# Optimization experiments

Measured on AMD Instinct MI355X. Metric: run time of the kernel, lower is better.

Reference implementation:

```python
import jax, jax.numpy as jnp
import numpy as np

B, S, D, H = 2, 2048, 1024, 16
HD = D // H  # head_dim = 64

def setup_inputs() -> dict:
    key = jax.random.key(0)
    ks = jax.random.split(key, 10)
    s = 1.0 / np.sqrt(D)
    return {
        "hidden_states": jax.random.normal(ks[0], (B, S, D), jnp.float32),
        "attention_mask": jnp.ones((B, S), jnp.float32),
        "q_w": jax.random.uniform(ks[1], (D, D), jnp.float32, -s, s),
        "q_b": jax.random.uniform(ks[2], (D,), jnp.float32, -s, s),
        "k_w": jax.random.uniform(ks[3], (D, D), jnp.float32, -s, s),
        "k_b": jax.random.uniform(ks[4], (D,), jnp.float32, -s, s),
        "v_w": jax.random.uniform(ks[5], (D, D), jnp.float32, -s, s),
        "v_b": jax.random.uniform(ks[6], (D,), jnp.float32, -s, s),
        "o_w": jax.random.uniform(ks[7], (D, D), jnp.float32, -s, s),
        "o_b": jax.random.uniform(ks[8], (D,), jnp.float32, -s, s),
    }

def reference(hidden_states, attention_mask, q_w, q_b, k_w, k_b, v_w, v_b, o_w, o_b):
    scale = HD ** -0.5
    # projections; torch Linear: x @ W^T + b. Here weights stored as (D, D) used directly.
    q = hidden_states @ q_w + q_b  # [B,S,D]
    k = hidden_states @ k_w + k_b
    v = hidden_states @ v_w + v_b
    # split heads -> [B,H,S,HD]
    q = q.reshape(B, S, H, HD).transpose(0, 2, 1, 3)
    k = k.reshape(B, S, H, HD).transpose(0, 2, 1, 3)
    v = v.reshape(B, S, H, HD).transpose(0, 2, 1, 3)
    scores = jnp.einsum('bhqd,bhkd->bhqk', q, k) * scale  # [B,H,S,S]
    # additive mask from 2D [B,S] mask (1=keep, 0=mask)
    scores = scores + (1.0 - attention_mask)[:, None, None, :] * -10000.0
    attn = jax.nn.softmax(scores, axis=-1)
    ctx = jnp.einsum('bhqk,bhkd->bhqd', attn, v)  # [B,H,S,HD]
    ctx = ctx.transpose(0, 2, 1, 3).reshape(B, S, D)
    return ctx @ o_w + o_b
```

## Files before the change

kernel.cpp:

```cpp
#include <hip/hip_runtime.h>
#include <hip/hip_bf16.h>

#define B_ 2
#define S_ 2048
#define D_ 1024
#define H_ 16
#define HD_ 64

#define QSCALE 0.18033688f
#define MLOG2E 14426.950408f

#define EXP2(x) __builtin_amdgcn_exp2f(x)

typedef __attribute__((ext_vector_type(8))) short bf16x8;
typedef __attribute__((ext_vector_type(4))) short short4v;
typedef __attribute__((ext_vector_type(4))) float floatx4;
typedef __attribute__((ext_vector_type(16))) float f32x16;

static __device__ __forceinline__ float bf2f(short u) {
  union { float f; unsigned int i; } c;
  c.i = ((unsigned int)(unsigned short)u) << 16;
  return c.f;
}
static __device__ __forceinline__ short f2bf(float f) {
  union { float f; unsigned int i; } c; c.f = f;
  unsigned int r = c.i + 0x7FFFu + ((c.i >> 16) & 1u);
  return (short)(r >> 16);
}

static __device__ __forceinline__ int cvtpk_bf16(float a, float b) {
  int r;
  asm("v_cvt_pk_bf16_f32 %0, %1, %2" : "=v"(r) : "v"(a), "v"(b));
  return r;
}
static __device__ __forceinline__ void swap32(int& a, int& b) {
  asm("v_permlane32_swap_b32 %0, %1" : "+v"(a), "+v"(b));
}

static __device__ __forceinline__ void gld_lds16(const void* g, void* l) {
  __builtin_amdgcn_global_load_lds(
      (const __attribute__((address_space(1))) unsigned int*)g,
      (__attribute__((address_space(3))) unsigned int*)l, 16, 0, 0);
}

__global__ __launch_bounds__(256)
void prep(const float* __restrict__ w0, const float* __restrict__ w1,
          const float* __restrict__ w2, const float* __restrict__ w3,
          const float* __restrict__ hs, short* __restrict__ WT,
          short* __restrict__ Xb) {
  const int z = blockIdx.z;
  if (z < 4) {
    __shared__ short t[64][65];
    const float* src = z == 0 ? w0 : z == 1 ? w1 : z == 2 ? w2 : w3;
    short* dst = WT + (size_t)z * D_ * D_;
    const int tx = threadIdx.x & 63, ty = threadIdx.x >> 6;
    const int r0 = blockIdx.y * 64, c0 = blockIdx.x * 64;
    for (int r = ty; r < 64; r += 4)
      t[r][tx] = f2bf(src[(size_t)(r0 + r) * D_ + c0 + tx]);
    __syncthreads();
    for (int r = ty; r < 64; r += 4)
      dst[(size_t)(c0 + r) * D_ + r0 + tx] = t[tx][r];
  } else {
    const int bid = blockIdx.y * 16 + blockIdx.x;
    const float4* in4 = (const float4*)hs;
    short4v* out4 = (short4v*)Xb;
#pragma unroll
    for (int i = 0; i < 16; i++) {
      const int idx = bid * 4096 + i * 256 + threadIdx.x;
      const float4 v = in4[idx];
      short4v o;
      o[0] = f2bf(v.x); o[1] = f2bf(v.y); o[2] = f2bf(v.z); o[3] = f2bf(v.w);
      out4[idx] = o;
    }
  }
}

__global__ __launch_bounds__(256, 2)
void gemm_qkv(const short* __restrict__ X, const short* __restrict__ WT,
              const float* __restrict__ qb, const float* __restrict__ kb,
              const float* __restrict__ vb,
              short* __restrict__ Qo, short* __restrict__ Ko,
              short* __restrict__ Vt) {
  __shared__ __align__(16) short As[128 * 32];
  __shared__ __align__(16) short Bs[128 * 32];
  const int tid = threadIdx.x;
  const int wave = tid >> 6, lane = tid & 63;
  const int col = lane & 15, quad = lane >> 4;
  const int m0 = blockIdx.x * 128;
  const int nt = blockIdx.y;
  const int widx = nt >> 3;
  const int n1 = (nt & 7) * 128;
  const short* Bsrc = WT + (size_t)widx * D_ * D_ + (size_t)n1 * D_;
  const int b = m0 >> 11;

  const int srow = tid >> 2;
  const int skcol = (tid & 3) * 8;
  const short* ga = X + (size_t)(m0 + srow) * D_ + skcol;
  const short* gb = Bsrc + (size_t)srow * D_ + skcol;
  short* la = As + tid * 8;
  short* lb = Bs + tid * 8;

  floatx4 acc[4][4];
#pragma unroll
  for (int i = 0; i < 4; i++)
#pragma unroll
    for (int j = 0; j < 4; j++) acc[i][j] = floatx4{0.f, 0.f, 0.f, 0.f};

  if (widx < 2) {
    const int wseq = (wave >> 1) * 64;
    const int wfeat = (wave & 1) * 64;
    for (int k0 = 0; k0 < D_; k0 += 32) {
      gld_lds16(ga, la);
      gld_lds16(ga + 64 * D_, la + 2048);
      gld_lds16(gb, lb);
      gld_lds16(gb + 64 * D_, lb + 2048);
      ga += 32; gb += 32;
      __syncthreads();
      bf16x8 xf[4], wf[4];
#pragma unroll
      for (int j = 0; j < 4; j++)
        xf[j] = *(const bf16x8*)(As + (wseq + j * 16 + col) * 32 + quad * 8);
#pragma unroll
      for (int i = 0; i < 4; i++)
        wf[i] = *(const bf16x8*)(Bs + (wfeat + i * 16 + col) * 32 + quad * 8);
#pragma unroll
      for (int i = 0; i < 4; i++)
#pragma unroll
        for (int j = 0; j < 4; j++)
          acc[i][j] = __builtin_amdgcn_mfma_f32_16x16x32_bf16(wf[i], xf[j],
                                                              acc[i][j], 0, 0, 0);
      __syncthreads();
    }
    const float* bias = widx == 0 ? qb : kb;
    short* dst = widx == 0 ? Qo : Ko;
    const float scale = widx == 0 ? QSCALE : 1.0f;
#pragma unroll
    for (int i = 0; i < 4; i++) {
      const int nf = n1 + wfeat + i * 16 + quad * 4;
      const int h = nf >> 6, hd = nf & 63;
      const float4 bv = *(const float4*)(bias + nf);
#pragma unroll
      for (int j = 0; j < 4; j++) {
        const int s = (m0 + wseq + j * 16 + col) & (S_ - 1);
        short4v pk;
        pk[0] = f2bf((acc[i][j][0] + bv.x) * scale);
        pk[1] = f2bf((acc[i][j][1] + bv.y) * scale);
        pk[2] = f2bf((acc[i][j][2] + bv.z) * scale);
        pk[3] = f2bf((acc[i][j][3] + bv.w) * scale);
        *(short4v*)(dst + ((size_t)(b * H_ + h) * S_ + s) * HD_ + hd) = pk;
      }
    }
  } else {
    const int wrow = (wave & 1) * 64;
    const int wcol = (wave >> 1) * 64;
    for (int k0 = 0; k0 < D_; k0 += 32) {
      gld_lds16(ga, la);
      gld_lds16(ga + 64 * D_, la + 2048);
      gld_lds16(gb, lb);
      gld_lds16(gb + 64 * D_, lb + 2048);
      ga += 32; gb += 32;
      __syncthreads();
      bf16x8 af[4], bfr[4];
#pragma unroll
      for (int i = 0; i < 4; i++)
        af[i] = *(const bf16x8*)(As + (wrow + i * 16 + col) * 32 + quad * 8);
#pragma unroll
      for (int j = 0; j < 4; j++)
        bfr[j] = *(const bf16x8*)(Bs + (wcol + j * 16 + col) * 32 + quad * 8);
#pragma unroll
      for (int i = 0; i < 4; i++)
#pragma unroll
        for (int j = 0; j < 4; j++)
          acc[i][j] = __builtin_amdgcn_mfma_f32_16x16x32_bf16(af[i], bfr[j],
                                                              acc[i][j], 0, 0, 0);
      __syncthreads();
    }
    float bv[4];
#pragma unroll
    for (int j = 0; j < 4; j++) bv[j] = vb[n1 + wcol + j * 16 + col];
#pragma unroll
    for (int i = 0; i < 4; i++) {
      const int s = (m0 + wrow + i * 16 + quad * 4) & (S_ - 1);
#pragma unroll
      for (int j = 0; j < 4; j++) {
        const int nl = n1 + wcol + j * 16 + col;
        const int h = nl >> 6, hd = nl & 63;
        short4v pk;
#pragma unroll
        for (int r = 0; r < 4; r++) pk[r] = f2bf(acc[i][j][r] + bv[j]);
        *(short4v*)(Vt + ((size_t)(b * H_ + h) * HD_ + hd) * S_ + s) = pk;
      }
    }
  }
}

__global__ __launch_bounds__(256, 2)
void attn(const short* __restrict__ Q, const short* __restrict__ K,
          const short* __restrict__ Vt, const float* __restrict__ mask,
          short* __restrict__ ctx) {
  __shared__ __align__(16) short Ks[2][4096];
  __shared__ __align__(16) short Vs[2][4096];
  __shared__ __align__(16) float Wb[S_];
  const int tid = threadIdx.x, wave = tid >> 6, lane = tid & 63;
  const int l31 = lane & 31, hi = lane >> 5, x7 = l31 & 7;
  const int lin = blockIdx.x;
  const int qt = (lin >> 3) & 15;
  const int gi = (lin & 7) + ((lin >> 7) << 3);
  const int h = gi & 15, b = gi >> 4;
  const short* Qh = Q + (size_t)(b * H_ + h) * S_ * HD_;
  const short* Kh = K + (size_t)(b * H_ + h) * S_ * HD_;
  const short* Vh = Vt + (size_t)(b * H_ + h) * HD_ * S_;
  const float* mk = mask + (size_t)b * S_;
  const int q0 = qt * 128 + wave * 32;

  const int r1 = tid >> 3, c1 = (tid & 7) ^ (r1 & 7);
  const int r2 = r1 + 32,  c2 = (tid & 7) ^ (r2 & 7);

  gld_lds16(Kh + (size_t)r1 * HD_ + c1 * 8, &Ks[0][tid * 8]);
  gld_lds16(Kh + (size_t)r2 * HD_ + c2 * 8, &Ks[0][(tid + 256) * 8]);
  gld_lds16(Vh + (size_t)r1 * S_ + c1 * 8, &Vs[0][tid * 8]);
  gld_lds16(Vh + (size_t)r2 * S_ + c2 * 8, &Vs[0][(tid + 256) * 8]);

  for (int i = tid; i < S_; i += 256)
    Wb[i] = (mk[i] - 1.0f) * MLOG2E;

  bf16x8 qf[4];
  {
    const short* qp = Qh + (size_t)(q0 + l31) * HD_ + hi * 8;
#pragma unroll
    for (int c = 0; c < 4; c++) qf[c] = *(const bf16x8*)(qp + c * 16);
  }

  bf16x8 ones;
#pragma unroll
  for (int i = 0; i < 8; i++) ones[i] = (short)0x3F80;

  f32x16 acc0, acc1, rsa;
#pragma unroll
  for (int r = 0; r < 16; r++) { acc0[r] = 0.f; acc1[r] = 0.f; rsa[r] = 0.f; }

  const int kbase = l31 * 64;
  int ko[4];
#pragma unroll
  for (int c = 0; c < 4; c++) ko[c] = ((((c << 1) | hi) ^ x7) << 3);

  __syncthreads();

  for (int it = 0; it < S_ / 64; it++) {
    const int buf = it & 1;
    const int kt = it * 64;
    if (it + 1 < S_ / 64) {
      const int kn = kt + 64;
      gld_lds16(Kh + (size_t)(kn + r1) * HD_ + c1 * 8, &Ks[buf ^ 1][tid * 8]);
      gld_lds16(Kh + (size_t)(kn + r2) * HD_ + c2 * 8, &Ks[buf ^ 1][(tid + 256) * 8]);
      gld_lds16(Vh + (size_t)r1 * S_ + kn + c1 * 8, &Vs[buf ^ 1][tid * 8]);
      gld_lds16(Vh + (size_t)r2 * S_ + kn + c2 * 8, &Vs[buf ^ 1][(tid + 256) * 8]);
    }

    bf16x8 pB[4];
#pragma unroll
    for (int t = 0; t < 2; t++) {
      const int kb2 = kt + t * 32 + 4 * hi;
      const float4 b0 = *(const float4*)&Wb[kb2];
      const float4 b1 = *(const float4*)&Wb[kb2 + 8];
      const float4 b2 = *(const float4*)&Wb[kb2 + 16];
      const float4 b3 = *(const float4*)&Wb[kb2 + 24];
      f32x16 z;
      z[0] = b0.x; z[1] = b0.y; z[2]  = b0.z; z[3]  = b0.w;
      z[4] = b1.x; z[5] = b1.y; z[6]  = b1.z; z[7]  = b1.w;
      z[8] = b2.x; z[9] = b2.y; z[10] = b2.z; z[11] = b2.w;
      z[12] = b3.x; z[13] = b3.y; z[14] = b3.z; z[15] = b3.w;
      const short* kp = &Ks[buf][t * 2048 + kbase];
#pragma unroll
      for (int c = 0; c < 4; c++) {
        const bf16x8 kf = *(const bf16x8*)(kp + ko[c]);
        z = __builtin_amdgcn_mfma_f32_32x32x16_bf16(kf, qf[c], z, 0, 0, 0);
      }
      float p[16];
#pragma unroll
      for (int r = 0; r < 16; r++) p[r] = EXP2(z[r]);
      int a0 = cvtpk_bf16(p[0], p[1]),   a1 = cvtpk_bf16(p[2], p[3]);
      int cc0 = cvtpk_bf16(p[4], p[5]),  cc1 = cvtpk_bf16(p[6], p[7]);
      int e0 = cvtpk_bf16(p[8], p[9]),   e1 = cvtpk_bf16(p[10], p[11]);
      int g0 = cvtpk_bf16(p[12], p[13]), g1 = cvtpk_bf16(p[14], p[15]);
      swap32(a0, cc0); swap32(a1, cc1);
      swap32(e0, g0);  swap32(e1, g1);
      union { int i[4]; bf16x8 v; } u0, u1;
      u0.i[0] = a0; u0.i[1] = a1; u0.i[2] = cc0; u0.i[3] = cc1;
      u1.i[0] = e0; u1.i[1] = e1; u1.i[2] = g0;  u1.i[3] = g1;
      pB[t * 2] = u0.v;
      pB[t * 2 + 1] = u1.v;
    }

#pragma unroll
    for (int kc = 0; kc < 4; kc++)
      rsa = __builtin_amdgcn_mfma_f32_32x32x16_bf16(ones, pB[kc], rsa, 0, 0, 0);

    const short* vp0 = &Vs[buf][kbase];
    const short* vp1 = &Vs[buf][2048 + kbase];
#pragma unroll
    for (int kc = 0; kc < 4; kc++) {
      const bf16x8 vf0 = *(const bf16x8*)(vp0 + ko[kc]);
      const bf16x8 vf1 = *(const bf16x8*)(vp1 + ko[kc]);
      acc0 = __builtin_amdgcn_mfma_f32_32x32x16_bf16(vf0, pB[kc], acc0, 0, 0, 0);
      acc1 = __builtin_amdgcn_mfma_f32_32x32x16_bf16(vf1, pB[kc], acc1, 0, 0, 0);
    }
    __syncthreads();
  }

  const float inv = 1.0f / (rsa[0] + 1e-30f);
  const size_t row = (size_t)b * S_ + q0 + l31;
#pragma unroll
  for (int g4 = 0; g4 < 4; g4++) {
    short4v o0, o1;
#pragma unroll
    for (int j = 0; j < 4; j++) {
      o0[j] = f2bf(acc0[g4 * 4 + j] * inv);
      o1[j] = f2bf(acc1[g4 * 4 + j] * inv);
    }
    short* cp = ctx + row * D_ + h * HD_ + g4 * 8 + 4 * hi;
    *(short4v*)(cp) = o0;
    *(short4v*)(cp + 32) = o1;
  }
}

__global__ __launch_bounds__(256, 2)
void gemm_out(const short* __restrict__ X, const short* __restrict__ WT,
              const float* __restrict__ ob, float* __restrict__ out) {
  __shared__ __align__(16) short As[64 * 32];
  __shared__ __align__(16) short Bs[128 * 32];
  const int tid = threadIdx.x;
  const int wave = tid >> 6, lane = tid & 63;
  const int col = lane & 15, quad = lane >> 4;
  const int m0 = blockIdx.x * 64;
  const int n0 = blockIdx.y * 128;
  const short* Bsrc = WT + (size_t)n0 * D_;
  const int wrow = (wave & 1) * 32;
  const int wcol = (wave >> 1) * 64;

  floatx4 acc[2][4];
#pragma unroll
  for (int i = 0; i < 2; i++)
#pragma unroll
    for (int j = 0; j < 4; j++) acc[i][j] = floatx4{0.f, 0.f, 0.f, 0.f};

  const int arow = tid >> 2, akcol = (tid & 3) * 8;
  const short* ga = X + (size_t)(m0 + arow) * D_ + akcol;
  const short* gb = Bsrc + (size_t)arow * D_ + akcol;
  short* la = As + tid * 8;
  short* lb = Bs + tid * 8;

  for (int k0 = 0; k0 < D_; k0 += 32) {
    gld_lds16(ga, la);
    gld_lds16(gb, lb);
    gld_lds16(gb + 64 * D_, lb + 2048);
    ga += 32; gb += 32;
    __syncthreads();
    bf16x8 af[2], bfr[4];
#pragma unroll
    for (int i = 0; i < 2; i++)
      af[i] = *(const bf16x8*)(As + (wrow + i * 16 + col) * 32 + quad * 8);
#pragma unroll
    for (int j = 0; j < 4; j++)
      bfr[j] = *(const bf16x8*)(Bs + (wcol + j * 16 + col) * 32 + quad * 8);
#pragma unroll
    for (int i = 0; i < 2; i++)
#pragma unroll
      for (int j = 0; j < 4; j++)
        acc[i][j] = __builtin_amdgcn_mfma_f32_16x16x32_bf16(af[i], bfr[j],
                                                            acc[i][j], 0, 0, 0);
    __syncthreads();
  }

  float bv[4];
#pragma unroll
  for (int j = 0; j < 4; j++) bv[j] = ob[n0 + wcol + j * 16 + col];

#pragma unroll
  for (int i = 0; i < 2; i++) {
    const int m = m0 + wrow + i * 16 + quad * 4;
#pragma unroll
    for (int j = 0; j < 4; j++) {
      const int n = n0 + wcol + j * 16 + col;
#pragma unroll
      for (int r = 0; r < 4; r++)
        out[(size_t)(m + r) * D_ + n] = acc[i][j][r] + bv[j];
    }
  }
}

extern "C" void kernel_launch(void* const* d_in, const int* in_sizes, int n_in,
                              void* d_out, int out_size, void* d_ws, size_t ws_size,
                              hipStream_t stream) {
  (void)in_sizes; (void)n_in; (void)out_size; (void)ws_size;
  const float* hs  = (const float*)d_in[0];
  const float* msk = (const float*)d_in[1];
  const float* qw  = (const float*)d_in[2];
  const float* qb  = (const float*)d_in[3];
  const float* kw  = (const float*)d_in[4];
  const float* kb  = (const float*)d_in[5];
  const float* vw  = (const float*)d_in[6];
  const float* vb  = (const float*)d_in[7];
  const float* ow  = (const float*)d_in[8];
  const float* ob  = (const float*)d_in[9];
  float* out = (float*)d_out;
  char* ws = (char*)d_ws;

  short* Xb  = (short*)(ws);
  short* WT  = (short*)(ws + (8ull  << 20));
  short* Qp  = (short*)(ws + (16ull << 20));
  short* Kp  = (short*)(ws + (24ull << 20));
  short* Vtp = (short*)(ws + (32ull << 20));
  short* Ctx = Xb;

  prep<<<dim3(16, 16, 5), 256, 0, stream>>>(qw, kw, vw, ow, hs, WT, Xb);
  gemm_qkv<<<dim3(32, 24), 256, 0, stream>>>(Xb, WT, qb, kb, vb, Qp, Kp, Vtp);
  attn<<<dim3(512), 256, 0, stream>>>(Qp, Kp, Vtp, msk, Ctx);
  gemm_out<<<dim3(64, 8), 256, 0, stream>>>(Ctx, WT + 3ull * D_ * D_, ob, out);
}
```

Measured before the change: 195.5 us.

## Shrink attention blocks to two waves, stagger KV start, add MFMA priority

```diff
diff --git a/kernel.cpp b/kernel.cpp
--- a/kernel.cpp
+++ b/kernel.cpp
@@ -17,11 +17,6 @@
 typedef __attribute__((ext_vector_type(4))) float floatx4;
 typedef __attribute__((ext_vector_type(16))) float f32x16;
 
-static __device__ __forceinline__ float bf2f(short u) {
-  union { float f; unsigned int i; } c;
-  c.i = ((unsigned int)(unsigned short)u) << 16;
-  return c.f;
-}
 static __device__ __forceinline__ short f2bf(float f) {
   union { float f; unsigned int i; } c; c.f = f;
   unsigned int r = c.i + 0x7FFFu + ((c.i >> 16) & 1u);
@@ -194,35 +189,38 @@
   }
 }
 
-__global__ __launch_bounds__(256, 2)
+__global__ __launch_bounds__(128, 2)
 void attn(const short* __restrict__ Q, const short* __restrict__ K,
           const short* __restrict__ Vt, const float* __restrict__ mask,
           short* __restrict__ ctx) {
   __shared__ __align__(16) short Ks[2][4096];
   __shared__ __align__(16) short Vs[2][4096];
-  __shared__ __align__(16) float Wb[S_];
   const int tid = threadIdx.x, wave = tid >> 6, lane = tid & 63;
   const int l31 = lane & 31, hi = lane >> 5, x7 = l31 & 7;
   const int lin = blockIdx.x;
-  const int qt = (lin >> 3) & 15;
-  const int gi = (lin & 7) + ((lin >> 7) << 3);
+  const int qt = (lin >> 3) & 31;
+  const int gi = (lin & 7) | ((lin >> 8) << 3);
   const int h = gi & 15, b = gi >> 4;
   const short* Qh = Q + (size_t)(b * H_ + h) * S_ * HD_;
   const short* Kh = K + (size_t)(b * H_ + h) * S_ * HD_;
   const short* Vh = Vt + (size_t)(b * H_ + h) * HD_ * S_;
   const float* mk = mask + (size_t)b * S_;
-  const int q0 = qt * 128 + wave * 32;
-
-  const int r1 = tid >> 3, c1 = (tid & 7) ^ (r1 & 7);
-  const int r2 = r1 + 32,  c2 = (tid & 7) ^ (r2 & 7);
-
-  gld_lds16(Kh + (size_t)r1 * HD_ + c1 * 8, &Ks[0][tid * 8]);
-  gld_lds16(Kh + (size_t)r2 * HD_ + c2 * 8, &Ks[0][(tid + 256) * 8]);
-  gld_lds16(Vh + (size_t)r1 * S_ + c1 * 8, &Vs[0][tid * 8]);
-  gld_lds16(Vh + (size_t)r2 * S_ + c2 * 8, &Vs[0][(tid + 256) * 8]);
-
-  for (int i = tid; i < S_; i += 256)
-    Wb[i] = (mk[i] - 1.0f) * MLOG2E;
+  const int q0 = qt * 64 + wave * 32;
+
+  int srow[4], schk[4];
+#pragma unroll
+  for (int i = 0; i < 4; i++) {
+    const int s = tid + i * 128;
+    srow[i] = s >> 3;
+    schk[i] = ((s & 7) ^ (srow[i] & 7)) * 8;
+  }
+
+  const int kt0 = qt * 64;
+#pragma unroll
+  for (int i = 0; i < 4; i++) {
+    gld_lds16(Kh + (size_t)(kt0 + srow[i]) * HD_ + schk[i], &Ks[0][(tid + i * 128) * 8]);
+    gld_lds16(Vh + (size_t)srow[i] * S_ + kt0 + schk[i], &Vs[0][(tid + i * 128) * 8]);
+  }
 
   bf16x8 qf[4];
   {
@@ -248,34 +246,43 @@
 
   for (int it = 0; it < S_ / 64; it++) {
     const int buf = it & 1;
-    const int kt = it * 64;
+    const int kt = ((it + qt) & 31) * 64;
     if (it + 1 < S_ / 64) {
-      const int kn = kt + 64;
-      gld_lds16(Kh + (size_t)(kn + r1) * HD_ + c1 * 8, &Ks[buf ^ 1][tid * 8]);
-      gld_lds16(Kh + (size_t)(kn + r2) * HD_ + c2 * 8, &Ks[buf ^ 1][(tid + 256) * 8]);
-      gld_lds16(Vh + (size_t)r1 * S_ + kn + c1 * 8, &Vs[buf ^ 1][tid * 8]);
-      gld_lds16(Vh + (size_t)r2 * S_ + kn + c2 * 8, &Vs[buf ^ 1][(tid + 256) * 8]);
+      const int kn = ((it + 1 + qt) & 31) * 64;
+#pragma unroll
+      for (int i = 0; i < 4; i++) {
+        gld_lds16(Kh + (size_t)(kn + srow[i]) * HD_ + schk[i],
+                  &Ks[buf ^ 1][(tid + i * 128) * 8]);
+        gld_lds16(Vh + (size_t)srow[i] * S_ + kn + schk[i],
+                  &Vs[buf ^ 1][(tid + i * 128) * 8]);
+      }
     }
 
     bf16x8 pB[4];
 #pragma unroll
     for (int t = 0; t < 2; t++) {
       const int kb2 = kt + t * 32 + 4 * hi;
-      const float4 b0 = *(const float4*)&Wb[kb2];
-      const float4 b1 = *(const float4*)&Wb[kb2 + 8];
-      const float4 b2 = *(const float4*)&Wb[kb2 + 16];
-      const float4 b3 = *(const float4*)&Wb[kb2 + 24];
+      const float4 b0 = *(const float4*)&mk[kb2];
+      const float4 b1 = *(const float4*)&mk[kb2 + 8];
+      const float4 b2 = *(const float4*)&mk[kb2 + 16];
+      const float4 b3 = *(const float4*)&mk[kb2 + 24];
       f32x16 z;
-      z[0] = b0.x; z[1] = b0.y; z[2]  = b0.z; z[3]  = b0.w;
-      z[4] = b1.x; z[5] = b1.y; z[6]  = b1.z; z[7]  = b1.w;
-      z[8] = b2.x; z[9] = b2.y; z[10] = b2.z; z[11] = b2.w;
-      z[12] = b3.x; z[13] = b3.y; z[14] = b3.z; z[15] = b3.w;
+      z[0]  = (b0.x - 1.0f) * MLOG2E; z[1]  = (b0.y - 1.0f) * MLOG2E;
+      z[2]  = (b0.z - 1.0f) * MLOG2E; z[3]  = (b0.w - 1.0f) * MLOG2E;
+      z[4]  = (b1.x - 1.0f) * MLOG2E; z[5]  = (b1.y - 1.0f) * MLOG2E;
+      z[6]  = (b1.z - 1.0f) * MLOG2E; z[7]  = (b1.w - 1.0f) * MLOG2E;
+      z[8]  = (b2.x - 1.0f) * MLOG2E; z[9]  = (b2.y - 1.0f) * MLOG2E;
+      z[10] = (b2.z - 1.0f) * MLOG2E; z[11] = (b2.w - 1.0f) * MLOG2E;
+      z[12] = (b3.x - 1.0f) * MLOG2E; z[13] = (b3.y - 1.0f) * MLOG2E;
+      z[14] = (b3.z - 1.0f) * MLOG2E; z[15] = (b3.w - 1.0f) * MLOG2E;
       const short* kp = &Ks[buf][t * 2048 + kbase];
+      __builtin_amdgcn_s_setprio(1);
 #pragma unroll
       for (int c = 0; c < 4; c++) {
         const bf16x8 kf = *(const bf16x8*)(kp + ko[c]);
         z = __builtin_amdgcn_mfma_f32_32x32x16_bf16(kf, qf[c], z, 0, 0, 0);
       }
+      __builtin_amdgcn_s_setprio(0);
       float p[16];
 #pragma unroll
       for (int r = 0; r < 16; r++) p[r] = EXP2(z[r]);
@@ -292,12 +299,12 @@
       pB[t * 2 + 1] = u1.v;
     }
 
+    const short* vp0 = &Vs[buf][kbase];
+    const short* vp1 = &Vs[buf][2048 + kbase];
+    __builtin_amdgcn_s_setprio(1);
 #pragma unroll
     for (int kc = 0; kc < 4; kc++)
       rsa = __builtin_amdgcn_mfma_f32_32x32x16_bf16(ones, pB[kc], rsa, 0, 0, 0);
-
-    const short* vp0 = &Vs[buf][kbase];
-    const short* vp1 = &Vs[buf][2048 + kbase];
 #pragma unroll
     for (int kc = 0; kc < 4; kc++) {
       const bf16x8 vf0 = *(const bf16x8*)(vp0 + ko[kc]);
@@ -305,6 +312,7 @@
       acc0 = __builtin_amdgcn_mfma_f32_32x32x16_bf16(vf0, pB[kc], acc0, 0, 0, 0);
       acc1 = __builtin_amdgcn_mfma_f32_32x32x16_bf16(vf1, pB[kc], acc1, 0, 0, 0);
     }
+    __builtin_amdgcn_s_setprio(0);
     __syncthreads();
   }
 
@@ -415,6 +423,6 @@
 
   prep<<<dim3(16, 16, 5), 256, 0, stream>>>(qw, kw, vw, ow, hs, WT, Xb);
   gemm_qkv<<<dim3(32, 24), 256, 0, stream>>>(Xb, WT, qb, kb, vb, Qp, Kp, Vtp);
-  attn<<<dim3(512), 256, 0, stream>>>(Qp, Kp, Vtp, msk, Ctx);
+  attn<<<dim3(1024), 128, 0, stream>>>(Qp, Kp, Vtp, msk, Ctx);
   gemm_out<<<dim3(64, 8), 256, 0, stream>>>(Ctx, WT + 3ull * D_ * D_, ob, out);
 }
```

Result: slower. 206.6 us (+5.7%).

## Split attention KV range in two and add a combine kernel

Applied to the files above, without the earlier changes.

```diff
diff --git a/kernel.cpp b/kernel.cpp
--- a/kernel.cpp
+++ b/kernel.cpp
@@ -17,11 +17,6 @@
 typedef __attribute__((ext_vector_type(4))) float floatx4;
 typedef __attribute__((ext_vector_type(16))) float f32x16;
 
-static __device__ __forceinline__ float bf2f(short u) {
-  union { float f; unsigned int i; } c;
-  c.i = ((unsigned int)(unsigned short)u) << 16;
-  return c.f;
-}
 static __device__ __forceinline__ short f2bf(float f) {
   union { float f; unsigned int i; } c; c.f = f;
   unsigned int r = c.i + 0x7FFFu + ((c.i >> 16) & 1u);
@@ -194,35 +189,46 @@
   }
 }
 
-__global__ __launch_bounds__(256, 2)
+__global__ __launch_bounds__(256, 4)
 void attn(const short* __restrict__ Q, const short* __restrict__ K,
           const short* __restrict__ Vt, const float* __restrict__ mask,
-          short* __restrict__ ctx) {
+          float* __restrict__ ctxP0, float* __restrict__ ctxP1,
+          float* __restrict__ rsP0, float* __restrict__ rsP1) {
   __shared__ __align__(16) short Ks[2][4096];
   __shared__ __align__(16) short Vs[2][4096];
-  __shared__ __align__(16) float Wb[S_];
+  __shared__ __align__(16) float Wb[1024];
   const int tid = threadIdx.x, wave = tid >> 6, lane = tid & 63;
   const int l31 = lane & 31, hi = lane >> 5, x7 = l31 & 7;
   const int lin = blockIdx.x;
-  const int qt = (lin >> 3) & 15;
-  const int gi = (lin & 7) + ((lin >> 7) << 3);
+  const int kh = (lin >> 3) & 1;
+  const int qt = (lin >> 4) & 15;
+  const int gi = (lin & 7) + ((lin >> 8) << 3);
   const int h = gi & 15, b = gi >> 4;
   const short* Qh = Q + (size_t)(b * H_ + h) * S_ * HD_;
   const short* Kh = K + (size_t)(b * H_ + h) * S_ * HD_;
   const short* Vh = Vt + (size_t)(b * H_ + h) * HD_ * S_;
   const float* mk = mask + (size_t)b * S_;
   const int q0 = qt * 128 + wave * 32;
-
-  const int r1 = tid >> 3, c1 = (tid & 7) ^ (r1 & 7);
-  const int r2 = r1 + 32,  c2 = (tid & 7) ^ (r2 & 7);
-
-  gld_lds16(Kh + (size_t)r1 * HD_ + c1 * 8, &Ks[0][tid * 8]);
-  gld_lds16(Kh + (size_t)r2 * HD_ + c2 * 8, &Ks[0][(tid + 256) * 8]);
-  gld_lds16(Vh + (size_t)r1 * S_ + c1 * 8, &Vs[0][tid * 8]);
-  gld_lds16(Vh + (size_t)r2 * S_ + c2 * 8, &Vs[0][(tid + 256) * 8]);
-
-  for (int i = tid; i < S_; i += 256)
-    Wb[i] = (mk[i] - 1.0f) * MLOG2E;
+  const int kk0 = kh * 1024;
+
+  int srow[2], schk[2];
+#pragma unroll
+  for (int i = 0; i < 2; i++) {
+    const int s = tid + i * 256;
+    srow[i] = s >> 3;
+    schk[i] = ((s & 7) ^ (srow[i] & 7)) * 8;
+  }
+
+#pragma unroll
+  for (int i = 0; i < 2; i++) {
+    gld_lds16(Kh + (size_t)(kk0 + srow[i]) * HD_ + schk[i],
+              &Ks[0][(tid + i * 256) * 8]);
+    gld_lds16(Vh + (size_t)srow[i] * S_ + kk0 + schk[i],
+              &Vs[0][(tid + i * 256) * 8]);
+  }
+
+  for (int i = tid; i < 1024; i += 256)
+    Wb[i] = (mk[kk0 + i] - 1.0f) * MLOG2E;
 
   bf16x8 qf[4];
   {
@@ -246,21 +252,24 @@
 
   __syncthreads();
 
-  for (int it = 0; it < S_ / 64; it++) {
+  for (int it = 0; it < 16; it++) {
     const int buf = it & 1;
-    const int kt = it * 64;
-    if (it + 1 < S_ / 64) {
-      const int kn = kt + 64;
-      gld_lds16(Kh + (size_t)(kn + r1) * HD_ + c1 * 8, &Ks[buf ^ 1][tid * 8]);
-      gld_lds16(Kh + (size_t)(kn + r2) * HD_ + c2 * 8, &Ks[buf ^ 1][(tid + 256) * 8]);
-      gld_lds16(Vh + (size_t)r1 * S_ + kn + c1 * 8, &Vs[buf ^ 1][tid * 8]);
-      gld_lds16(Vh + (size_t)r2 * S_ + kn + c2 * 8, &Vs[buf ^ 1][(tid + 256) * 8]);
+    const int ktl = it * 64;
+    if (it + 1 < 16) {
+      const int kn = kk0 + ktl + 64;
+#pragma unroll
+      for (int i = 0; i < 2; i++) {
+        gld_lds16(Kh + (size_t)(kn + srow[i]) * HD_ + schk[i],
+                  &Ks[buf ^ 1][(tid + i * 256) * 8]);
+        gld_lds16(Vh + (size_t)srow[i] * S_ + kn + schk[i],
+                  &Vs[buf ^ 1][(tid + i * 256) * 8]);
+      }
     }
 
     bf16x8 pB[4];
 #pragma unroll
     for (int t = 0; t < 2; t++) {
-      const int kb2 = kt + t * 32 + 4 * hi;
+      const int kb2 = ktl + t * 32 + 4 * hi;
       const float4 b0 = *(const float4*)&Wb[kb2];
       const float4 b1 = *(const float4*)&Wb[kb2 + 8];
       const float4 b2 = *(const float4*)&Wb[kb2 + 16];
@@ -271,11 +280,13 @@
       z[8] = b2.x; z[9] = b2.y; z[10] = b2.z; z[11] = b2.w;
       z[12] = b3.x; z[13] = b3.y; z[14] = b3.z; z[15] = b3.w;
       const short* kp = &Ks[buf][t * 2048 + kbase];
+      __builtin_amdgcn_s_setprio(1);
 #pragma unroll
       for (int c = 0; c < 4; c++) {
         const bf16x8 kf = *(const bf16x8*)(kp + ko[c]);
         z = __builtin_amdgcn_mfma_f32_32x32x16_bf16(kf, qf[c], z, 0, 0, 0);
       }
+      __builtin_amdgcn_s_setprio(0);
       float p[16];
 #pragma unroll
       for (int r = 0; r < 16; r++) p[r] = EXP2(z[r]);
@@ -292,12 +303,12 @@
       pB[t * 2 + 1] = u1.v;
     }
 
+    const short* vp0 = &Vs[buf][kbase];
+    const short* vp1 = &Vs[buf][2048 + kbase];
+    __builtin_amdgcn_s_setprio(1);
 #pragma unroll
     for (int kc = 0; kc < 4; kc++)
       rsa = __builtin_amdgcn_mfma_f32_32x32x16_bf16(ones, pB[kc], rsa, 0, 0, 0);
-
-    const short* vp0 = &Vs[buf][kbase];
-    const short* vp1 = &Vs[buf][2048 + kbase];
 #pragma unroll
     for (int kc = 0; kc < 4; kc++) {
       const bf16x8 vf0 = *(const bf16x8*)(vp0 + ko[kc]);
@@ -305,23 +316,51 @@
       acc0 = __builtin_amdgcn_mfma_f32_32x32x16_bf16(vf0, pB[kc], acc0, 0, 0, 0);
       acc1 = __builtin_amdgcn_mfma_f32_32x32x16_bf16(vf1, pB[kc], acc1, 0, 0, 0);
     }
+    __builtin_amdgcn_s_setprio(0);
     __syncthreads();
   }
 
-  const float inv = 1.0f / (rsa[0] + 1e-30f);
+  float* ctxP = kh ? ctxP1 : ctxP0;
+  float* rsP  = kh ? rsP1  : rsP0;
   const size_t row = (size_t)b * S_ + q0 + l31;
 #pragma unroll
   for (int g4 = 0; g4 < 4; g4++) {
-    short4v o0, o1;
-#pragma unroll
-    for (int j = 0; j < 4; j++) {
-      o0[j] = f2bf(acc0[g4 * 4 + j] * inv);
-      o1[j] = f2bf(acc1[g4 * 4 + j] * inv);
-    }
-    short* cp = ctx + row * D_ + h * HD_ + g4 * 8 + 4 * hi;
-    *(short4v*)(cp) = o0;
-    *(short4v*)(cp + 32) = o1;
-  }
+    float* cp = ctxP + row * D_ + h * HD_ + g4 * 8 + 4 * hi;
+    *(float4*)(cp) = make_float4(acc0[g4 * 4 + 0], acc0[g4 * 4 + 1],
+                                 acc0[g4 * 4 + 2], acc0[g4 * 4 + 3]);
+    *(float4*)(cp + 32) = make_float4(acc1[g4 * 4 + 0], acc1[g4 * 4 + 1],
+                                      acc1[g4 * 4 + 2], acc1[g4 * 4 + 3]);
+  }
+  if (hi == 0)
+    rsP[(size_t)(b * H_ + h) * S_ + q0 + l31] = rsa[0];
+}
+
+__global__ __launch_bounds__(256)
+void combine(const float* __restrict__ P0, const float* __restrict__ P1,
+             const float* __restrict__ rs0, const float* __restrict__ rs1,
+             short* __restrict__ ctx) {
+  const int t = blockIdx.x * 256 + threadIdx.x;
+  const int row = t >> 7;
+  const int dq = (t & 127) * 8;
+  const int b = row >> 11, s = row & (S_ - 1);
+  const int h = dq >> 6;
+  const size_t base = (size_t)row * D_ + dq;
+  const float4 a0 = *(const float4*)(P0 + base);
+  const float4 a1 = *(const float4*)(P0 + base + 4);
+  const float4 c0 = *(const float4*)(P1 + base);
+  const float4 c1 = *(const float4*)(P1 + base + 4);
+  const size_t ri = (size_t)(b * H_ + h) * S_ + s;
+  const float inv = 1.0f / (rs0[ri] + rs1[ri] + 1e-30f);
+  union { short sh[8]; int4 v; } o;
+  o.sh[0] = f2bf((a0.x + c0.x) * inv);
+  o.sh[1] = f2bf((a0.y + c0.y) * inv);
+  o.sh[2] = f2bf((a0.z + c0.z) * inv);
+  o.sh[3] = f2bf((a0.w + c0.w) * inv);
+  o.sh[4] = f2bf((a1.x + c1.x) * inv);
+  o.sh[5] = f2bf((a1.y + c1.y) * inv);
+  o.sh[6] = f2bf((a1.z + c1.z) * inv);
+  o.sh[7] = f2bf((a1.w + c1.w) * inv);
+  *(int4*)(ctx + base) = o.v;
 }
 
 __global__ __launch_bounds__(256, 2)
@@ -406,15 +445,20 @@
   float* out = (float*)d_out;
   char* ws = (char*)d_ws;
 
-  short* Xb  = (short*)(ws);
-  short* WT  = (short*)(ws + (8ull  << 20));
-  short* Qp  = (short*)(ws + (16ull << 20));
-  short* Kp  = (short*)(ws + (24ull << 20));
-  short* Vtp = (short*)(ws + (32ull << 20));
-  short* Ctx = Xb;
+  short* Xb   = (short*)(ws);
+  short* WT   = (short*)(ws + (8ull  << 20));
+  short* Qp   = (short*)(ws + (16ull << 20));
+  short* Kp   = (short*)(ws + (24ull << 20));
+  short* Vtp  = (short*)(ws + (32ull << 20));
+  float* ctxP0 = (float*)(ws + (40ull << 20));
+  float* ctxP1 = (float*)(ws + (56ull << 20));
+  float* rsP0  = (float*)(ws + (72ull << 20));
+  float* rsP1  = (float*)(ws + (73ull << 20));
+  short* Ctx  = Xb;
 
   prep<<<dim3(16, 16, 5), 256, 0, stream>>>(qw, kw, vw, ow, hs, WT, Xb);
   gemm_qkv<<<dim3(32, 24), 256, 0, stream>>>(Xb, WT, qb, kb, vb, Qp, Kp, Vtp);
-  attn<<<dim3(512), 256, 0, stream>>>(Qp, Kp, Vtp, msk, Ctx);
+  attn<<<dim3(1024), 256, 0, stream>>>(Qp, Kp, Vtp, msk, ctxP0, ctxP1, rsP0, rsP1);
+  combine<<<dim3(2048), 256, 0, stream>>>(ctxP0, ctxP1, rsP0, rsP1, Ctx);
   gemm_out<<<dim3(64, 8), 256, 0, stream>>>(Ctx, WT + 3ull * D_ * D_, ob, out);
 }
```

Result: no change. 196.8 us (+0.7%).
